# Kernel optimization log

Measured on AMD Instinct MI355X. Metric: run time of the kernel, lower is better.

## Reference

```python
import jax, jax.numpy as jnp
import numpy as np

B = 16
TOP_N = 4
IOU_THRESH = 0.25
PAD = 224
OUT = 224  # part image size
NUM_CLASSES = 200


def _gen_anchors(input_shape=(448, 448)):
    # Faithful port of NTSNet._generate_default_anchor_maps -> edge anchors,
    # then +PAD shift and int cast as in NTSNet.__init__.
    scales = [2.0 ** (1.0 / 3.0), 2.0 ** (2.0 / 3.0)]
    ratios = [0.667, 1.0, 1.5]
    settings = [(32, 48, scales), (64, 96, scales), (128, 192, [1.0] + scales)]
    edge = []
    for stride, size, scs in settings:
        H = int(np.ceil(input_shape[0] / stride))
        W = int(np.ceil(input_shape[1] / stride))
        ostart = stride / 2.0
        oy = np.arange(ostart, ostart + stride * H, stride).reshape(H, 1)
        ox = np.arange(ostart, ostart + stride * W, stride).reshape(1, W)
        cy = np.broadcast_to(oy, (H, W)).astype(np.float32)
        cx = np.broadcast_to(ox, (H, W)).astype(np.float32)
        for s in scs:
            for ar in ratios:
                h = size * s / float(ar) ** 0.5
                w = size * s * float(ar) ** 0.5
                e = np.stack([cy - h / 2.0, cx - w / 2.0, cy + h / 2.0, cx + w / 2.0], axis=-1)
                edge.append(e.reshape(-1, 4))
    edge = np.concatenate(edge, axis=0).astype(np.float32)
    return (edge + PAD).astype(np.int64).astype(np.int32)  # [1614,4] (y0,x0,y1,x1)


def _conv(x, w, b, stride, pad):
    y = jax.lax.conv_general_dilated(
        x, w, window_strides=(stride, stride),
        padding=[(pad, pad), (pad, pad)],
        dimension_numbers=("NCHW", "OIHW", "NCHW"))
    return y + b[None, :, None, None]


def _nms_single(scores, boxes, areas):
    # Hard NMS, fixed TOP_N iterations (jit-friendly): iteratively take the
    # highest-score box and suppress boxes with IoU >= IOU_THRESH.
    valid = jnp.ones(scores.shape, dtype=bool)
    picked = []
    for _ in range(TOP_N):
        i = jnp.argmax(jnp.where(valid, scores, -jnp.inf))
        b = boxes[i]
        ih = jnp.minimum(boxes[:, 2], b[2]) - jnp.maximum(boxes[:, 0], b[0])
        iw = jnp.minimum(boxes[:, 3], b[3]) - jnp.maximum(boxes[:, 1], b[1])
        inter = jnp.where((ih < 0) | (iw < 0), 0.0, ih * iw)
        iou = inter / (areas + areas[i] - inter)
        valid = valid & (iou < IOU_THRESH)
        picked.append(i)
    return jnp.stack(picked)  # [TOP_N]


def _crop_resize(img, box):
    # Bilinear resize of img[:, y0:y1, x0:x1] to OUTxOUT, align_corners=True
    # (matches F.interpolate(..., mode='bilinear', align_corners=True)).
    y0, x0, y1, x1 = box[0], box[1], box[2], box[3]
    h = (y1 - y0).astype(jnp.float32)
    w = (x1 - x0).astype(jnp.float32)
    t = jnp.arange(OUT, dtype=jnp.float32)
    sy = t * (h - 1.0) / (OUT - 1.0)
    sx = t * (w - 1.0) / (OUT - 1.0)
    fy = jnp.floor(sy)
    fx = jnp.floor(sx)
    wy = (sy - fy)[None, :, None]  # broadcast over rows
    wx = (sx - fx)[None, None, :]  # broadcast over cols
    iy0 = y0 + fy.astype(jnp.int32)
    ix0 = x0 + fx.astype(jnp.int32)
    iy1 = jnp.minimum(iy0 + 1, y1 - 1)
    ix1 = jnp.minimum(ix0 + 1, x1 - 1)
    r0 = img[:, iy0]  # [3,OUT,896]
    r1 = img[:, iy1]
    top = r0[:, :, ix0] * (1.0 - wx) + r0[:, :, ix1] * wx
    bot = r1[:, :, ix0] * (1.0 - wx) + r1[:, :, ix1] * wx
    return top * (1.0 - wy) + bot * wy  # [3,OUT,OUT]


def setup_inputs() -> dict:
    key = jax.random.key(0)
    ks = jax.random.split(key, 10)
    s = 0.02
    inp = {
        "x": jax.random.normal(ks[0], (B, 3, 448, 448), jnp.float32),
        "bb_w": jax.random.normal(ks[1], (2048, 3, 32, 32), jnp.float32) * s,
        "bb_b": jnp.zeros((2048,), jnp.float32),
        "n1_dw": jax.random.normal(ks[2], (128, 2048, 3, 3), jnp.float32) * s,
        "n1_db": jnp.zeros((128,), jnp.float32),
        "n1_tw": jax.random.normal(ks[3], (6, 128, 1, 1), jnp.float32) * s,
        "n1_tb": jnp.zeros((6,), jnp.float32),
        "n2_dw": jax.random.normal(ks[4], (128, 128, 3, 3), jnp.float32) * s,
        "n2_db": jnp.zeros((128,), jnp.float32),
        "n2_tw": jax.random.normal(ks[5], (6, 128, 1, 1), jnp.float32) * s,
        "n2_tb": jnp.zeros((6,), jnp.float32),
        "n3_dw": jax.random.normal(ks[6], (128, 128, 3, 3), jnp.float32) * s,
        "n3_db": jnp.zeros((128,), jnp.float32),
        "n3_tw": jax.random.normal(ks[7], (9, 128, 1, 1), jnp.float32) * s,
        "n3_tb": jnp.zeros((9,), jnp.float32),
        "cn_w": jax.random.normal(ks[8], (NUM_CLASSES, 10240), jnp.float32) * s,
        "cn_b": jnp.zeros((NUM_CLASSES,), jnp.float32),
        "anchors": jnp.asarray(_gen_anchors()),
    }
    return inp


def reference(x, bb_w, bb_b, n1_dw, n1_db, n1_tw, n1_tb, n2_dw, n2_db, n2_tw,
              n2_tb, n3_dw, n3_db, n3_tw, n3_tb, cn_w, cn_b, anchors):
    batch = x.shape[0]
    # Backbone -> raw pre-features [B,2048,14,14]
    raw = _conv(x, bb_w, bb_b, stride=32, pad=0)
    # Navigator unit -> rpn scores [B,1614]
    y1 = jax.nn.relu(_conv(raw, n1_dw, n1_db, 1, 1))            # [B,128,14,14]
    t1 = _conv(y1, n1_tw, n1_tb, 1, 0).reshape(batch, -1)        # [B,1176]
    y2 = jax.nn.relu(_conv(y1, n2_dw, n2_db, 2, 1))              # [B,128,7,7]
    t2 = _conv(y2, n2_tw, n2_tb, 1, 0).reshape(batch, -1)        # [B,294]
    y3 = jax.nn.relu(_conv(y2, n3_dw, n3_db, 2, 1))              # [B,128,4,4]
    t3 = _conv(y3, n3_tw, n3_tb, 1, 0).reshape(batch, -1)        # [B,144]
    rpn_score = jnp.concatenate([t1, t2, t3], axis=1)            # [B,1614]

    boxes_f = anchors.astype(jnp.float32)
    areas = (boxes_f[:, 2] - boxes_f[:, 0]) * (boxes_f[:, 3] - boxes_f[:, 1])
    top_idx = jax.vmap(_nms_single, in_axes=(0, None, None))(rpn_score, boxes_f, areas)  # [B,TOP_N]

    x_pad = jnp.pad(x, ((0, 0), (0, 0), (PAD, PAD), (PAD, PAD)))  # [B,3,896,896]
    sel_boxes = anchors[top_idx]                                  # [B,TOP_N,4]
    part_imgs = jax.vmap(lambda img, bs: jax.vmap(_crop_resize, in_axes=(None, 0))(img, bs))(
        x_pad, sel_boxes)                                         # [B,TOP_N,3,224,224]
    part_imgs = jax.lax.stop_gradient(part_imgs).reshape(batch * TOP_N, 3, OUT, OUT)

    # Shared backbone + tail (global avg pool; dropout is identity in eval)
    part_features = _conv(part_imgs, bb_w, bb_b, 32, 0).mean(axis=(2, 3))  # [B*TOP_N,2048]
    part_feature = part_features.reshape(batch, TOP_N, -1)[:, :4].reshape(batch, -1)  # num_cat=4
    raw_features = jax.lax.stop_gradient(raw).mean(axis=(2, 3))            # [B,2048]

    concat_out = jnp.concatenate([part_feature, raw_features], axis=1)     # [B,10240]
    concat_logits = concat_out @ cn_w.T + cn_b
    return concat_logits
```

## Files before the change

### kernel.cpp

```cpp
#include <hip/hip_runtime.h>
#include <cstdint>
#include <math.h>

typedef _Float16 half_t;
typedef __attribute__((ext_vector_type(8))) _Float16 half8;
typedef __attribute__((ext_vector_type(4))) float floatx4;


typedef __attribute__((address_space(3))) unsigned int lds_u32;
typedef const __attribute__((address_space(1))) unsigned int glb_u32;
__device__ __forceinline__ void glds16(const void* g, void* l) {
    __builtin_amdgcn_global_load_lds((glb_u32*)g, (lds_u32*)l, 16, 0, 0);
}

__global__ __launch_bounds__(256)
void prep_all(const float* __restrict__ x, const float* __restrict__ bbw,
              const float* __restrict__ n1dw, const float* __restrict__ n2dw,
              const float* __restrict__ n3dw, const float* __restrict__ cnb,
              const float* __restrict__ bbb,
              half_t* __restrict__ xh,
              half_t* __restrict__ bh, half_t* __restrict__ w1h,
              float* __restrict__ wt2t, float* __restrict__ wt3t,
              float* __restrict__ out, float* __restrict__ zpad,
              float* __restrict__ concat)
{
    const long t = (long)blockIdx.x * 256 + threadIdx.x;
    if (t < 1228800) {
        const int m = (int)(t % 3200), k8 = (int)(t / 3200);
        const int mt = m >> 7, mr = m & 127, s = k8 >> 2, kg = k8 & 3;
        const size_t dst = (((size_t)(mt * 96 + s) * 4 + kg) * 128 + mr) * 8;
        float f[8];
        if (m < 3136) {
            const int bq = m / 196, pos = m % 196, oy = pos / 14, ox = pos % 14;
            const int k = k8 * 8, c = k >> 10, r = (k >> 5) & 31, cc = k & 31;
            const float* p = x + ((size_t)(bq * 3 + c) * 448 + oy * 32 + r) * 448 + ox * 32 + cc;
            *(float4*)&f[0] = *(const float4*)p;
            *(float4*)&f[4] = *(const float4*)(p + 4);
        } else {
            #pragma unroll
            for (int j = 0; j < 8; ++j) f[j] = 0.f;
        }
        half8 h;
        #pragma unroll
        for (int j = 0; j < 8; ++j) h[j] = (half_t)f[j];
        *(half8*)(xh + dst) = h;
    } else if (t < 2015232) {
        const int t2 = (int)(t - 1228800);
        const int n = t2 / 384, k8 = t2 % 384;
        const float* p = bbw + (size_t)n * 3072 + k8 * 8;
        float f[8];
        *(float4*)&f[0] = *(const float4*)p;
        *(float4*)&f[4] = *(const float4*)(p + 4);
        const int nt = n >> 6, nr = n & 63, s = k8 >> 2, kg = k8 & 3;
        const size_t dst = (((size_t)(nt * 96 + s) * 4 + kg) * 64 + nr) * 8;
        half8 h;
        #pragma unroll
        for (int j = 0; j < 8; ++j) h[j] = (half_t)f[j];
        *(half8*)(bh + dst) = h;
    } else if (t < 2048000) {
        const int t2 = (int)(t - 2015232);
        const int n = t2 >> 8, ic8 = t2 & 255;
        const int s = ic8 >> 2, kg = ic8 & 3;
        const float* src = n1dw + ((size_t)n * 2048 + ic8 * 8) * 9;
        float buf[72];
        #pragma unroll
        for (int i = 0; i < 18; ++i) *(float4*)&buf[i * 4] = *(const float4*)(src + i * 4);
        #pragma unroll
        for (int tap = 0; tap < 9; ++tap) {
            half8 h;
            #pragma unroll
            for (int j = 0; j < 8; ++j) h[j] = (half_t)buf[j * 9 + tap];
            const size_t dst = (((size_t)(tap * 64 + s) * 4 + kg) * 128 + n) * 8;
            *(half8*)(w1h + dst) = h;
        }
    } else if (t < 2195456) {
        const int t2 = (int)(t - 2048000);
        const int oc = t2 % 128, rest = t2 / 128, ic = rest % 128, tap = rest / 128;
        wt2t[(tap * 128 + ic) * 128 + oc] = n2dw[((size_t)oc * 128 + ic) * 9 + tap];
    } else if (t < 2342912) {
        const int t2 = (int)(t - 2195456);
        const int oc = t2 % 128, rest = t2 / 128, ic = rest % 128, tap = rest / 128;
        wt3t[(tap * 128 + ic) * 128 + oc] = n3dw[((size_t)oc * 128 + ic) * 9 + tap];
    } else if (t < 2346112) {
        const int i = (int)(t - 2342912);
        out[i] = cnb[i % 200];
    } else if (t < 2346368) {
        zpad[t - 2346112] = 0.f;
    } else if (t < 2510208) {
        const int i = (int)(t - 2346368);
        const int r = i % 10240;
        concat[i] = (r < 8192) ? bbb[r & 2047] : 0.f;
    }
}

__global__ __launch_bounds__(256)
void gemm_x(const half_t* __restrict__ Ah, const half_t* __restrict__ Bh,
            const float* __restrict__ bias, half_t* __restrict__ outh)
{
    __shared__ __align__(16) char L[16384];
    const int tid = threadIdx.x, lane = tid & 63, wv = tid >> 6;
    const int nt = blockIdx.x, mt = blockIdx.y;
    const int lm = lane & 15, quad = lane >> 4;
    const int wm = wv >> 1, wn = wv & 1;

    const char* gAh = (const char*)Ah + (size_t)mt * 96 * 8192 + lane * 16;
    const int bhalf = wv >> 1, bkg = (wv & 1) * 2;
    const char* gB = (const char*)Bh + (size_t)(2 * nt + bhalf) * 96 * 4096 + bkg * 1024 + lane * 16;

    int afo[4], bfo[4];
    #pragma unroll
    for (int i = 0; i < 4; ++i) afo[i] = quad * 2048 + (wm * 64 + i * 16 + lm) * 16;
    #pragma unroll
    for (int j = 0; j < 4; ++j) bfo[j] = 8192 + wn * 4096 + quad * 1024 + (j * 16 + lm) * 16;

    floatx4 acc[4][4];
    const floatx4 fz = {0.f, 0.f, 0.f, 0.f};
    #pragma unroll
    for (int i = 0; i < 4; ++i)
        #pragma unroll
        for (int j = 0; j < 4; ++j) acc[i][j] = fz;

    for (int s = 0; s < 96; ++s) {
        const size_t sa = (size_t)s * 8192;
        glds16(gAh + sa + (2 * wv) * 1024,     L + (2 * wv) * 1024);
        glds16(gAh + sa + (2 * wv + 1) * 1024, L + (2 * wv + 1) * 1024);
        glds16(gB + (size_t)s * 4096,          L + 8192 + bhalf * 4096 + bkg * 1024);
        glds16(gB + (size_t)s * 4096 + 1024,   L + 8192 + bhalf * 4096 + (bkg + 1) * 1024);
        __syncthreads();
        half8 ah[4], bh[4];
        #pragma unroll
        for (int i = 0; i < 4; ++i) ah[i] = *(const half8*)(L + afo[i]);
        #pragma unroll
        for (int j = 0; j < 4; ++j) bh[j] = *(const half8*)(L + bfo[j]);
        #pragma unroll
        for (int i = 0; i < 4; ++i)
            #pragma unroll
            for (int j = 0; j < 4; ++j)
                acc[i][j] = __builtin_amdgcn_mfma_f32_16x16x32_f16(ah[i], bh[j], acc[i][j], 0, 0, 0);
        __syncthreads();
    }
    #pragma unroll
    for (int i = 0; i < 4; ++i) {
        const int m0 = mt * 128 + wm * 64 + i * 16 + quad * 4;
        #pragma unroll
        for (int j = 0; j < 4; ++j) {
            const int n = nt * 128 + wn * 64 + j * 16 + lm;
            const float bv = bias[n];
            #pragma unroll
            for (int r = 0; r < 4; ++r) {
                const int mm = m0 + r;
                if (mm < 3136)
                    outh[(size_t)mm * 2048 + n] = (half_t)(acc[i][j][r] + bv);
            }
        }
    }
}

__global__ __launch_bounds__(256)
void gemm_nav(const half_t* __restrict__ rawh, const half_t* __restrict__ Bh,
              const char* __restrict__ zpad, float* __restrict__ y1p)
{
    __shared__ __align__(16) char L[16384];
    const int tid = threadIdx.x, lane = tid & 63, wv = tid >> 6;
    const int tx = blockIdx.x;
    const int tap = tx >> 1, ks = tx & 1;
    const int mt = blockIdx.y;
    const int lm = lane & 15, quad = lane >> 4;
    const int wm = wv >> 1, wn = wv & 1;

    const char* baseH[2];
    int stp[2];
    #pragma unroll
    for (int rh = 0; rh < 2; ++rh) {
        const int grow = mt * 128 + rh * 64 + lane;
        const int b = grow / 196, pos = grow % 196, oy = pos / 14, ox = pos % 14;
        const int iy = oy + tap / 3 - 1, ix = ox + tap % 3 - 1;
        const bool av = (grow < 3136) && iy >= 0 && iy < 14 && ix >= 0 && ix < 14;
        const size_t rowoff = av ? ((size_t)(b * 196 + iy * 14 + ix)) * 4096 + ks * 2048 + wv * 16 : 0;
        baseH[rh] = av ? (const char*)rawh + rowoff : zpad;
        stp[rh] = av ? 64 : 0;
    }
    const char* gB = (const char*)Bh + (size_t)tap * 524288 + (size_t)ks * 32 * 8192 + lane * 16;

    int afo[4], bfo[4];
    #pragma unroll
    for (int i = 0; i < 4; ++i) afo[i] = quad * 2048 + (wm * 64 + i * 16 + lm) * 16;
    #pragma unroll
    for (int j = 0; j < 4; ++j) bfo[j] = 8192 + quad * 2048 + (wn * 64 + j * 16 + lm) * 16;

    floatx4 acc[4][4];
    const floatx4 fz = {0.f, 0.f, 0.f, 0.f};
    #pragma unroll
    for (int i = 0; i < 4; ++i)
        #pragma unroll
        for (int j = 0; j < 4; ++j) acc[i][j] = fz;

    for (int s = 0; s < 32; ++s) {
        glds16(baseH[0] + s * stp[0], L + wv * 2048);
        glds16(baseH[1] + s * stp[1], L + wv * 2048 + 1024);
        glds16(gB + (size_t)s * 8192 + (2 * wv) * 1024,     L + 8192 + (2 * wv) * 1024);
        glds16(gB + (size_t)s * 8192 + (2 * wv + 1) * 1024, L + 8192 + (2 * wv + 1) * 1024);
        __syncthreads();
        half8 ah[4], bh[4];
        #pragma unroll
        for (int i = 0; i < 4; ++i) ah[i] = *(const half8*)(L + afo[i]);
        #pragma unroll
        for (int j = 0; j < 4; ++j) bh[j] = *(const half8*)(L + bfo[j]);
        #pragma unroll
        for (int i = 0; i < 4; ++i)
            #pragma unroll
            for (int j = 0; j < 4; ++j)
                acc[i][j] = __builtin_amdgcn_mfma_f32_16x16x32_f16(ah[i], bh[j], acc[i][j], 0, 0, 0);
        __syncthreads();
    }
    #pragma unroll
    for (int i = 0; i < 4; ++i) {
        const int m0 = mt * 128 + wm * 64 + i * 16 + quad * 4;
        #pragma unroll
        for (int j = 0; j < 4; ++j) {
            const int n = wn * 64 + j * 16 + lm;
            #pragma unroll
            for (int r = 0; r < 4; ++r) {
                const int mm = m0 + r;
                if (mm < 3136)
                    y1p[((size_t)tx * 3136 + mm) * 128 + n] = acc[i][j][r];
            }
        }
    }
}

__global__ __launch_bounds__(256)
void y1r_rm(const float* __restrict__ y1p, const float* __restrict__ bias,
            float* __restrict__ y1,
            const half_t* __restrict__ rh, float* __restrict__ concat)
{
    if (blockIdx.x < 1568) {
        const int t = blockIdx.x * 256 + threadIdx.x;
        const int n = t & 127;
        float s = bias[n];
        #pragma unroll
        for (int ks = 0; ks < 18; ++ks) s += y1p[(size_t)ks * 3136 * 128 + t];
        y1[t] = fmaxf(s, 0.f);
    } else {
        const int t = (blockIdx.x - 1568) * 256 + threadIdx.x;
        const int n = t & 2047, b = (t >> 11) & 15, pc = t >> 15;
        float s = 0.f;
        const int p0 = pc * 49;
        for (int p = p0; p < p0 + 49; ++p)
            s += (float)rh[(size_t)(b * 196 + p) * 2048 + n];
        atomicAdd(concat + (size_t)b * 10240 + 8192 + n, s * (1.f / 196.f));
    }
}

__global__ __launch_bounds__(256)
void tidy_all(const float* __restrict__ y1, const float* __restrict__ y2,
              const float* __restrict__ y3,
              const float* __restrict__ w1, const float* __restrict__ b1,
              const float* __restrict__ w2, const float* __restrict__ b2,
              const float* __restrict__ w3, const float* __restrict__ b3,
              float* __restrict__ scores)
{
    const int wid = (blockIdx.x * 256 + threadIdx.x) >> 6;
    const int lane = threadIdx.x & 63;
    if (wid >= 16 * 1614) return;
    const int b = wid / 1614, idx = wid % 1614;
    const float* in; const float* w; const float* bi; int ch;
    if (idx < 1176) {
        ch = idx / 196; in = y1 + (size_t)(b * 196 + idx % 196) * 128; w = w1; bi = b1;
    } else if (idx < 1470) {
        const int i2 = idx - 1176;
        ch = i2 / 49; in = y2 + (size_t)(b * 49 + i2 % 49) * 128; w = w2; bi = b2;
    } else {
        const int i3 = idx - 1470;
        ch = i3 / 16; in = y3 + (size_t)(b * 16 + i3 % 16) * 128; w = w3; bi = b3;
    }
    const float* wr = w + ch * 128;
    float acc = in[lane] * wr[lane] + in[lane + 64] * wr[lane + 64];
    #pragma unroll
    for (int s = 32; s > 0; s >>= 1) acc += __shfl_down(acc, s, 64);
    if (lane == 0) scores[b * 1614 + idx] = acc + bi[ch];
}

__global__ __launch_bounds__(256)
void conv_s2(const float* __restrict__ in, const float* __restrict__ wt,
             const float* __restrict__ bias, float* __restrict__ out,
             int Win, int Wout)
{
    const int t = blockIdx.x * 256 + threadIdx.x;
    const int oc = t & 127;
    const int pos = (t >> 7) % (Wout * Wout);
    const int b = t / (128 * Wout * Wout);
    if (b >= 16) return;
    const int oy = pos / Wout, ox = pos % Wout;
    float acc = bias[oc];
    for (int dy = 0; dy < 3; ++dy) {
        const int y = oy * 2 + dy - 1;
        if (y < 0 || y >= Win) continue;
        for (int dx = 0; dx < 3; ++dx) {
            const int x = ox * 2 + dx - 1;
            if (x < 0 || x >= Win) continue;
            const float* ip = in + (size_t)(b * Win * Win + y * Win + x) * 128;
            const float* wp = wt + (size_t)(dy * 3 + dx) * 16384 + oc;
            for (int ic = 0; ic < 128; ++ic)
                acc += ip[ic] * wp[ic * 128];
        }
    }
    out[(size_t)(b * Wout * Wout + pos) * 128 + oc] = fmaxf(acc, 0.f);
}

__global__ __launch_bounds__(256)
void nms(const float* __restrict__ scores, const int* __restrict__ anchors,
         int* __restrict__ top_idx)
{
    __shared__ float wv_v[4];
    __shared__ int wv_i[4];
    __shared__ int s_pick;
    const int b = blockIdx.x, tid = threadIdx.x;
    const int lane = tid & 63, wv = tid >> 6;
    float sc[7], ay0[7], ax0[7], ay1[7], ax1[7];
    unsigned int vmask = 0;
    #pragma unroll
    for (int j = 0; j < 7; ++j) {
        const int i = tid + j * 256;
        if (i < 1614) {
            sc[j]  = scores[b * 1614 + i];
            ay0[j] = (float)anchors[i * 4 + 0];
            ax0[j] = (float)anchors[i * 4 + 1];
            ay1[j] = (float)anchors[i * 4 + 2];
            ax1[j] = (float)anchors[i * 4 + 3];
            vmask |= 1u << j;
        }
    }
    for (int r = 0; r < 4; ++r) {
        float bv = -INFINITY; int bi = 0x7fffffff;
        #pragma unroll
        for (int j = 0; j < 7; ++j) {
            if (vmask & (1u << j)) {
                const float v = sc[j];
                const int i = tid + j * 256;
                if (v > bv || (v == bv && i < bi)) { bv = v; bi = i; }
            }
        }
        #pragma unroll
        for (int s = 32; s > 0; s >>= 1) {
            const float v2 = __shfl_down(bv, s, 64);
            const int   i2 = __shfl_down(bi, s, 64);
            if (v2 > bv || (v2 == bv && i2 < bi)) { bv = v2; bi = i2; }
        }
        if (lane == 0) { wv_v[wv] = bv; wv_i[wv] = bi; }
        __syncthreads();
        if (tid == 0) {
            float fv = wv_v[0]; int fi = wv_i[0];
            #pragma unroll
            for (int k = 1; k < 4; ++k)
                if (wv_v[k] > fv || (wv_v[k] == fv && wv_i[k] < fi)) { fv = wv_v[k]; fi = wv_i[k]; }
            s_pick = fi;
            top_idx[b * 4 + r] = fi;
        }
        __syncthreads();
        const int pick = s_pick;
        const float py0 = (float)anchors[pick * 4 + 0], px0 = (float)anchors[pick * 4 + 1];
        const float py1 = (float)anchors[pick * 4 + 2], px1 = (float)anchors[pick * 4 + 3];
        const float pa = (py1 - py0) * (px1 - px0);
        #pragma unroll
        for (int j = 0; j < 7; ++j) {
            if (vmask & (1u << j)) {
                const float ih = fminf(ay1[j], py1) - fmaxf(ay0[j], py0);
                const float iw = fminf(ax1[j], px1) - fmaxf(ax0[j], px0);
                const float inter = (ih < 0.f || iw < 0.f) ? 0.f : ih * iw;
                const float area = (ay1[j] - ay0[j]) * (ax1[j] - ax0[j]);
                const float iou = inter / ((area + pa) - inter);
                if (iou >= 0.25f) vmask &= ~(1u << j);
            }
        }
    }
}

__global__ __launch_bounds__(256)
void crop_mean(const float* __restrict__ x, const int* __restrict__ anchors,
               const int* __restrict__ top_idx, float* __restrict__ abar)
{
    __shared__ float red[256];
    const int bi = blockIdx.x;
    const int q = bi / 96, rem = bi % 96, c = rem >> 5, r = rem & 31;
    const int tid = threadIdx.x;
    const int cc = tid & 31, ps = tid >> 5;
    const int idx = top_idx[q];
    const int y0 = anchors[idx * 4 + 0], x0 = anchors[idx * 4 + 1];
    const int y1 = anchors[idx * 4 + 2], x1 = anchors[idx * 4 + 3];
    const float hh = (float)(y1 - y0), ww = (float)(x1 - x0);
    const float* xb = x + (size_t)((q >> 2) * 3 + c) * 200704;
    float acc = 0.f;
    for (int p = ps; p < 49; p += 8) {
        const int oy = p / 7, ox = p % 7;
        const int typ = oy * 32 + r;
        const int txp = ox * 32 + cc;
        const float sy = (float)typ * (hh - 1.0f) / 223.0f;
        const float fy = floorf(sy);
        const float wy = sy - fy;
        const int iy0 = y0 + (int)fy;
        const int iy1 = min(iy0 + 1, y1 - 1);
        const float sx = (float)txp * (ww - 1.0f) / 223.0f;
        const float fx = floorf(sx);
        const float wx = sx - fx;
        const int ix0 = x0 + (int)fx;
        const int ix1 = min(ix0 + 1, x1 - 1);
        const int ry0 = iy0 - 224, ry1 = iy1 - 224;
        const int rx0 = ix0 - 224, rx1 = ix1 - 224;
        const bool vy0 = (ry0 >= 0 && ry0 < 448), vy1 = (ry1 >= 0 && ry1 < 448);
        const bool vx0 = (rx0 >= 0 && rx0 < 448), vx1 = (rx1 >= 0 && rx1 < 448);
        const float v00 = (vy0 && vx0) ? xb[(size_t)ry0 * 448 + rx0] : 0.f;
        const float v01 = (vy0 && vx1) ? xb[(size_t)ry0 * 448 + rx1] : 0.f;
        const float v10 = (vy1 && vx0) ? xb[(size_t)ry1 * 448 + rx0] : 0.f;
        const float v11 = (vy1 && vx1) ? xb[(size_t)ry1 * 448 + rx1] : 0.f;
        const float top = v00 * (1.f - wx) + v01 * wx;
        const float bot = v10 * (1.f - wx) + v11 * wx;
        acc += top * (1.f - wy) + bot * wy;
    }
    red[tid] = acc;
    __syncthreads();
    if (tid < 32) {
        float s = 0.f;
        #pragma unroll
        for (int k = 0; k < 8; ++k) s += red[tid + 32 * k];
        abar[(size_t)q * 3072 + c * 1024 + r * 32 + cc] = s * (1.f / 49.f);
    }
}

__global__ __launch_bounds__(256)
void part_gemm(const float* __restrict__ abar, const half_t* __restrict__ Bh,
               float* __restrict__ concat)
{
    __shared__ __align__(16) char L[12288];
    const int tid = threadIdx.x, lane = tid & 63, wv = tid >> 6;
    const int lm = lane & 15, quad = lane >> 4;
    const int nt = blockIdx.x, ks = blockIdx.y;
    const char* gBh = (const char*)Bh + ((size_t)nt * 96 + ks * 12) * 4096 + lane * 16;
    const int am = tid & 63, akg = tid >> 6;

    floatx4 acc[4], accl[4];
    const floatx4 fz = {0.f, 0.f, 0.f, 0.f};
    #pragma unroll
    for (int j = 0; j < 4; ++j) { acc[j] = fz; accl[j] = fz; }

    for (int s = 0; s < 12; ++s) {
        {
            const float* pa = abar + (size_t)am * 3072 + (ks * 12 + s) * 32 + akg * 8;
            float f[8];
            *(float4*)&f[0] = *(const float4*)pa;
            *(float4*)&f[4] = *(const float4*)(pa + 4);
            half8 h, l;
            #pragma unroll
            for (int j = 0; j < 8; ++j) {
                const half_t hh = (half_t)f[j];
                h[j] = hh;
                l[j] = (half_t)(f[j] - (float)hh);
            }
            *(half8*)(L + (akg * 64 + am) * 16) = h;
            *(half8*)(L + 4096 + (akg * 64 + am) * 16) = l;
        }
        glds16(gBh + (size_t)s * 4096 + wv * 1024, L + 8192 + wv * 1024);
        __syncthreads();
        half8 ah, al, bh[4];
        ah = *(const half8*)(L + (quad * 64 + wv * 16 + lm) * 16);
        al = *(const half8*)(L + 4096 + (quad * 64 + wv * 16 + lm) * 16);
        #pragma unroll
        for (int j = 0; j < 4; ++j) bh[j] = *(const half8*)(L + 8192 + (quad * 64 + j * 16 + lm) * 16);
        #pragma unroll
        for (int j = 0; j < 4; ++j) {
            acc[j]  = __builtin_amdgcn_mfma_f32_16x16x32_f16(ah, bh[j], acc[j], 0, 0, 0);
            accl[j] = __builtin_amdgcn_mfma_f32_16x16x32_f16(al, bh[j], accl[j], 0, 0, 0);
        }
        __syncthreads();
    }
    #pragma unroll
    for (int j = 0; j < 4; ++j) {
        const int n = nt * 64 + j * 16 + lm;
        #pragma unroll
        for (int r = 0; r < 4; ++r) {
            const int m = wv * 16 + quad * 4 + r;
            atomicAdd(concat + (size_t)(m >> 2) * 10240 + (m & 3) * 2048 + n,
                      acc[j][r] + accl[j][r]);
        }
    }
}

__global__ __launch_bounds__(256)
void cls_gemm(const float* __restrict__ concat, const float* __restrict__ w,
              float* __restrict__ out)
{
    __shared__ float ws_[8 * 321];
    __shared__ float cs_[16 * 321];
    __shared__ float red[256];
    const int nchunk = blockIdx.x, ks = blockIdx.y;
    const int tid = threadIdx.x;
    for (int i = tid; i < 2560; i += 256) {
        const int r = i / 320, k = i % 320;
        ws_[r * 321 + k] = w[(size_t)(nchunk * 8 + r) * 10240 + ks * 320 + k];
    }
    for (int i = tid; i < 5120; i += 256) {
        const int r = i / 320, k = i % 320;
        cs_[r * 321 + k] = concat[(size_t)r * 10240 + ks * 320 + k];
    }
    __syncthreads();
    const int b = tid & 15, c = (tid >> 4) & 7, hf = tid >> 7;
    const float* cp = cs_ + b * 321 + hf * 160;
    const float* wp = ws_ + c * 321 + hf * 160;
    float a = 0.f;
    #pragma unroll 8
    for (int k = 0; k < 160; ++k) a += cp[k] * wp[k];
    red[tid] = a;
    __syncthreads();
    if (tid < 128) atomicAdd(out + b * 200 + nchunk * 8 + c, red[tid] + red[tid + 128]);
}

extern "C" void kernel_launch(void* const* d_in, const int* in_sizes, int n_in,
                              void* d_out, int out_size, void* d_ws, size_t ws_size,
                              hipStream_t stream)
{
    const float* x     = (const float*)d_in[0];
    const float* bb_w  = (const float*)d_in[1];
    const float* bb_b  = (const float*)d_in[2];
    const float* n1_dw = (const float*)d_in[3];
    const float* n1_db = (const float*)d_in[4];
    const float* n1_tw = (const float*)d_in[5];
    const float* n1_tb = (const float*)d_in[6];
    const float* n2_dw = (const float*)d_in[7];
    const float* n2_db = (const float*)d_in[8];
    const float* n2_tw = (const float*)d_in[9];
    const float* n2_tb = (const float*)d_in[10];
    const float* n3_dw = (const float*)d_in[11];
    const float* n3_db = (const float*)d_in[12];
    const float* n3_tw = (const float*)d_in[13];
    const float* n3_tb = (const float*)d_in[14];
    const float* cn_w  = (const float*)d_in[15];
    const float* cn_b  = (const float*)d_in[16];
    const int*   anchors = (const int*)d_in[17];
    float* out = (float*)d_out;
    char* W = (char*)d_ws;

    half_t* bbwh  = (half_t*)(W + 0);
    float*  zpad  = (float*)(W + 12582912);
    int*    topidx= (int*)(W + 12583936);
    float*  scores= (float*)(W + 12584960);
    float*  y1    = (float*)(W + 12688384);
    float*  y2    = (float*)(W + 14294016);
    float*  y3    = (float*)(W + 14695424);
    float*  concat= (float*)(W + 14826496);
    half_t* w1h   = (half_t*)(W + 15481856);
    float*  wt2t  = (float*)(W + 20200448);
    float*  wt3t  = (float*)(W + 20790272);
    char* E = W + 21380096;
    half_t* xh    = (half_t*)E;
    float*  y1p   = (float*)E;
    char* F = W + 60701696;
    half_t* rawh  = (half_t*)F;
    float*  abar  = (float*)F;

    prep_all<<<9806, 256, 0, stream>>>(x, bb_w, n1_dw, n2_dw, n3_dw, cn_b, bb_b,
                                       xh, bbwh, w1h, wt2t, wt3t, out, zpad, concat);

    gemm_x<<<dim3(16, 25), 256, 0, stream>>>(xh, bbwh, bb_b, rawh);
    gemm_nav<<<dim3(18, 25), 256, 0, stream>>>(rawh, w1h, (const char*)zpad, y1p);
    y1r_rm<<<2080, 256, 0, stream>>>(y1p, n1_db, y1, rawh, concat);

    conv_s2<<<392, 256, 0, stream>>>(y1, wt2t, n2_db, y2, 14, 7);
    conv_s2<<<128, 256, 0, stream>>>(y2, wt3t, n3_db, y3, 7, 4);
    tidy_all<<<6456, 256, 0, stream>>>(y1, y2, y3, n1_tw, n1_tb, n2_tw, n2_tb,
                                       n3_tw, n3_tb, scores);

    nms<<<16, 256, 0, stream>>>(scores, anchors, topidx);
    crop_mean<<<6144, 256, 0, stream>>>(x, anchors, topidx, abar);

    part_gemm<<<dim3(32, 8), 256, 0, stream>>>(abar, bbwh, concat);
    cls_gemm<<<dim3(25, 32), 256, 0, stream>>>(concat, cn_w, out);
}
```

Baseline: 409.6 us.

## Shrink GEMM M-tile to 64 rows and fuse tidy scoring into stride-2 convs

Both the backbone GEMM and the navigator 3x3 GEMM move from 128x128 tiles to 64x128 tiles, with each wave owning 16 rows and 8 N-fragments. Each iteration now covers two K-steps of MFMA with a larger LDS buffer. Since 3136 = 49*64, the grids grow from 25 to 49 M-tiles, which gives more blocks to spread across CUs and drops the row-bound checks. Separately, the per-scale tidy score dot products are folded into the conv kernels and a small tidy3 kernel. This lets score work overlap with the convs instead of running after all of them, at the cost of less per-block operand reuse in the GEMMs.

```diff
diff --git a/kernel.cpp b/kernel.cpp
--- a/kernel.cpp
+++ b/kernel.cpp
@@ -97,62 +97,56 @@
 void gemm_x(const half_t* __restrict__ Ah, const half_t* __restrict__ Bh,
             const float* __restrict__ bias, half_t* __restrict__ outh)
 {
-    __shared__ __align__(16) char L[16384];
+    __shared__ __align__(16) char L[24576];
     const int tid = threadIdx.x, lane = tid & 63, wv = tid >> 6;
     const int nt = blockIdx.x, mt = blockIdx.y;
     const int lm = lane & 15, quad = lane >> 4;
-    const int wm = wv >> 1, wn = wv & 1;
-
-    const char* gAh = (const char*)Ah + (size_t)mt * 96 * 8192 + lane * 16;
-    const int bhalf = wv >> 1, bkg = (wv & 1) * 2;
-    const char* gB = (const char*)Bh + (size_t)(2 * nt + bhalf) * 96 * 4096 + bkg * 1024 + lane * 16;
-
-    int afo[4], bfo[4];
-    #pragma unroll
-    for (int i = 0; i < 4; ++i) afo[i] = quad * 2048 + (wm * 64 + i * 16 + lm) * 16;
-    #pragma unroll
-    for (int j = 0; j < 4; ++j) bfo[j] = 8192 + wn * 4096 + quad * 1024 + (j * 16 + lm) * 16;
-
-    floatx4 acc[4][4];
+
+    const char* gA = (const char*)Ah + (size_t)(mt >> 1) * 786432 + (mt & 1) * 1024 + lane * 16;
+    const char* gB = (const char*)Bh + (size_t)(2 * nt) * 393216 + lane * 16;
+
+    const int a0 = 2 * wv, a1 = 2 * wv + 1;
+    const int aof0 = (a0 >> 2) * 4096 + (a0 & 3) * 1024;
+    const int aog0 = (a0 >> 2) * 8192 + (a0 & 3) * 2048;
+    const int aof1 = (a1 >> 2) * 4096 + (a1 & 3) * 1024;
+    const int aog1 = (a1 >> 2) * 8192 + (a1 & 3) * 2048;
+    const int bsi = wv >> 1, bnh = wv & 1;
+    const size_t bgb = (size_t)bnh * 393216 + bsi * 4096;
+    const int blb = 8192 + (bsi * 2 + bnh) * 4096;
+
+    floatx4 acc[8];
     const floatx4 fz = {0.f, 0.f, 0.f, 0.f};
     #pragma unroll
-    for (int i = 0; i < 4; ++i)
-        #pragma unroll
-        for (int j = 0; j < 4; ++j) acc[i][j] = fz;
-
-    for (int s = 0; s < 96; ++s) {
-        const size_t sa = (size_t)s * 8192;
-        glds16(gAh + sa + (2 * wv) * 1024,     L + (2 * wv) * 1024);
-        glds16(gAh + sa + (2 * wv + 1) * 1024, L + (2 * wv + 1) * 1024);
-        glds16(gB + (size_t)s * 4096,          L + 8192 + bhalf * 4096 + bkg * 1024);
-        glds16(gB + (size_t)s * 4096 + 1024,   L + 8192 + bhalf * 4096 + (bkg + 1) * 1024);
-        __syncthreads();
-        half8 ah[4], bh[4];
-        #pragma unroll
-        for (int i = 0; i < 4; ++i) ah[i] = *(const half8*)(L + afo[i]);
-        #pragma unroll
-        for (int j = 0; j < 4; ++j) bh[j] = *(const half8*)(L + bfo[j]);
+    for (int j = 0; j < 8; ++j) acc[j] = fz;
+
+    for (int s = 0; s < 48; ++s) {
+        const size_t sa = (size_t)(2 * s) * 8192;
+        const size_t sb = (size_t)(2 * s) * 4096;
+        glds16(gA + sa + aog0, L + aof0);
+        glds16(gA + sa + aog1, L + aof1);
         #pragma unroll
         for (int i = 0; i < 4; ++i)
+            glds16(gB + bgb + sb + i * 1024, L + blb + i * 1024);
+        __syncthreads();
+        #pragma unroll
+        for (int ki = 0; ki < 2; ++ki) {
+            half8 a = *(const half8*)(L + ki * 4096 + quad * 1024 + (wv * 16 + lm) * 16);
             #pragma unroll
-            for (int j = 0; j < 4; ++j)
-                acc[i][j] = __builtin_amdgcn_mfma_f32_16x16x32_f16(ah[i], bh[j], acc[i][j], 0, 0, 0);
-        __syncthreads();
-    }
-    #pragma unroll
-    for (int i = 0; i < 4; ++i) {
-        const int m0 = mt * 128 + wm * 64 + i * 16 + quad * 4;
-        #pragma unroll
-        for (int j = 0; j < 4; ++j) {
-            const int n = nt * 128 + wn * 64 + j * 16 + lm;
-            const float bv = bias[n];
-            #pragma unroll
-            for (int r = 0; r < 4; ++r) {
-                const int mm = m0 + r;
-                if (mm < 3136)
-                    outh[(size_t)mm * 2048 + n] = (half_t)(acc[i][j][r] + bv);
+            for (int j = 0; j < 8; ++j) {
+                half8 b = *(const half8*)(L + 8192 + (ki * 2 + (j >> 2)) * 4096 + quad * 1024 + ((j & 3) * 16 + lm) * 16);
+                acc[j] = __builtin_amdgcn_mfma_f32_16x16x32_f16(a, b, acc[j], 0, 0, 0);
             }
         }
+        __syncthreads();
+    }
+    const int m0 = mt * 64 + wv * 16 + quad * 4;
+    #pragma unroll
+    for (int j = 0; j < 8; ++j) {
+        const int n = nt * 128 + j * 16 + lm;
+        const float bv = bias[n];
+        #pragma unroll
+        for (int r = 0; r < 4; ++r)
+            outh[(size_t)(m0 + r) * 2048 + n] = (half_t)(acc[j][r] + bv);
     }
 }
 
@@ -160,72 +154,59 @@
 void gemm_nav(const half_t* __restrict__ rawh, const half_t* __restrict__ Bh,
               const char* __restrict__ zpad, float* __restrict__ y1p)
 {
-    __shared__ __align__(16) char L[16384];
+    __shared__ __align__(16) char L[24576];
     const int tid = threadIdx.x, lane = tid & 63, wv = tid >> 6;
     const int tx = blockIdx.x;
     const int tap = tx >> 1, ks = tx & 1;
     const int mt = blockIdx.y;
     const int lm = lane & 15, quad = lane >> 4;
-    const int wm = wv >> 1, wn = wv & 1;
-
-    const char* baseH[2];
-    int stp[2];
-    #pragma unroll
-    for (int rh = 0; rh < 2; ++rh) {
-        const int grow = mt * 128 + rh * 64 + lane;
-        const int b = grow / 196, pos = grow % 196, oy = pos / 14, ox = pos % 14;
-        const int iy = oy + tap / 3 - 1, ix = ox + tap % 3 - 1;
-        const bool av = (grow < 3136) && iy >= 0 && iy < 14 && ix >= 0 && ix < 14;
-        const size_t rowoff = av ? ((size_t)(b * 196 + iy * 14 + ix)) * 4096 + ks * 2048 + wv * 16 : 0;
-        baseH[rh] = av ? (const char*)rawh + rowoff : zpad;
-        stp[rh] = av ? 64 : 0;
-    }
-    const char* gB = (const char*)Bh + (size_t)tap * 524288 + (size_t)ks * 32 * 8192 + lane * 16;
-
-    int afo[4], bfo[4];
-    #pragma unroll
-    for (int i = 0; i < 4; ++i) afo[i] = quad * 2048 + (wm * 64 + i * 16 + lm) * 16;
-    #pragma unroll
-    for (int j = 0; j < 4; ++j) bfo[j] = 8192 + quad * 2048 + (wn * 64 + j * 16 + lm) * 16;
-
-    floatx4 acc[4][4];
+
+    const int grow = mt * 64 + lane;
+    const int b = grow / 196, pos = grow % 196, oy = pos / 14, ox = pos % 14;
+    const int iy = oy + tap / 3 - 1, ix = ox + tap % 3 - 1;
+    const bool av = (iy >= 0 && iy < 14 && ix >= 0 && ix < 14);
+    const char* abase = av ? (const char*)rawh + ((size_t)(b * 196 + iy * 14 + ix)) * 4096 + ks * 2048 : zpad;
+    const int stp = av ? 1 : 0;
+
+    const int a0 = 2 * wv, a1 = 2 * wv + 1;
+    const int ac0 = (a0 >> 2) * 64 + (a0 & 3) * 16, al0 = (a0 >> 2) * 4096 + (a0 & 3) * 1024;
+    const int ac1 = (a1 >> 2) * 64 + (a1 & 3) * 16, al1 = (a1 >> 2) * 4096 + (a1 & 3) * 1024;
+    const int bsi = wv >> 1, bnh = wv & 1;
+    const char* gB = (const char*)Bh + (size_t)tap * 524288 + (size_t)(ks * 32) * 8192 + bnh * 1024 + lane * 16;
+    const int blb = 8192 + bsi * 8192 + bnh * 1024;
+
+    floatx4 acc[8];
     const floatx4 fz = {0.f, 0.f, 0.f, 0.f};
     #pragma unroll
-    for (int i = 0; i < 4; ++i)
-        #pragma unroll
-        for (int j = 0; j < 4; ++j) acc[i][j] = fz;
-
-    for (int s = 0; s < 32; ++s) {
-        glds16(baseH[0] + s * stp[0], L + wv * 2048);
-        glds16(baseH[1] + s * stp[1], L + wv * 2048 + 1024);
-        glds16(gB + (size_t)s * 8192 + (2 * wv) * 1024,     L + 8192 + (2 * wv) * 1024);
-        glds16(gB + (size_t)s * 8192 + (2 * wv + 1) * 1024, L + 8192 + (2 * wv + 1) * 1024);
-        __syncthreads();
-        half8 ah[4], bh[4];
-        #pragma unroll
-        for (int i = 0; i < 4; ++i) ah[i] = *(const half8*)(L + afo[i]);
-        #pragma unroll
-        for (int j = 0; j < 4; ++j) bh[j] = *(const half8*)(L + bfo[j]);
+    for (int j = 0; j < 8; ++j) acc[j] = fz;
+
+    for (int s = 0; s < 16; ++s) {
+        const int rowo = s * 128;
+        glds16(abase + stp * (rowo + ac0), L + al0);
+        glds16(abase + stp * (rowo + ac1), L + al1);
+        const size_t sb = (size_t)(2 * s + bsi) * 8192;
         #pragma unroll
         for (int i = 0; i < 4; ++i)
+            glds16(gB + sb + i * 2048, L + blb + i * 2048);
+        __syncthreads();
+        #pragma unroll
+        for (int ki = 0; ki < 2; ++ki) {
+            half8 a = *(const half8*)(L + ki * 4096 + quad * 1024 + (wv * 16 + lm) * 16);
             #pragma unroll
-            for (int j = 0; j < 4; ++j)
-                acc[i][j] = __builtin_amdgcn_mfma_f32_16x16x32_f16(ah[i], bh[j], acc[i][j], 0, 0, 0);
-        __syncthreads();
-    }
-    #pragma unroll
-    for (int i = 0; i < 4; ++i) {
-        const int m0 = mt * 128 + wm * 64 + i * 16 + quad * 4;
-        #pragma unroll
-        for (int j = 0; j < 4; ++j) {
-            const int n = wn * 64 + j * 16 + lm;
-            #pragma unroll
-            for (int r = 0; r < 4; ++r) {
-                const int mm = m0 + r;
-                if (mm < 3136)
-                    y1p[((size_t)tx * 3136 + mm) * 128 + n] = acc[i][j][r];
+            for (int j = 0; j < 8; ++j) {
+                half8 bq = *(const half8*)(L + 8192 + ki * 8192 + quad * 2048 + (j * 16 + lm) * 16);
+                acc[j] = __builtin_amdgcn_mfma_f32_16x16x32_f16(a, bq, acc[j], 0, 0, 0);
             }
         }
+        __syncthreads();
+    }
+    const int m0 = mt * 64 + wv * 16 + quad * 4;
+    #pragma unroll
+    for (int j = 0; j < 8; ++j) {
+        const int n = j * 16 + lm;
+        #pragma unroll
+        for (int r = 0; r < 4; ++r)
+            y1p[((size_t)tx * 3136 + m0 + r) * 128 + n] = acc[j][r];
     }
 }
 
@@ -252,41 +233,20 @@
     }
 }
 
-__global__ __launch_bounds__(256)
-void tidy_all(const float* __restrict__ y1, const float* __restrict__ y2,
-              const float* __restrict__ y3,
-              const float* __restrict__ w1, const float* __restrict__ b1,
-              const float* __restrict__ w2, const float* __restrict__ b2,
-              const float* __restrict__ w3, const float* __restrict__ b3,
-              float* __restrict__ scores)
-{
-    const int wid = (blockIdx.x * 256 + threadIdx.x) >> 6;
-    const int lane = threadIdx.x & 63;
-    if (wid >= 16 * 1614) return;
-    const int b = wid / 1614, idx = wid % 1614;
-    const float* in; const float* w; const float* bi; int ch;
-    if (idx < 1176) {
-        ch = idx / 196; in = y1 + (size_t)(b * 196 + idx % 196) * 128; w = w1; bi = b1;
-    } else if (idx < 1470) {
-        const int i2 = idx - 1176;
-        ch = i2 / 49; in = y2 + (size_t)(b * 49 + i2 % 49) * 128; w = w2; bi = b2;
-    } else {
-        const int i3 = idx - 1470;
-        ch = i3 / 16; in = y3 + (size_t)(b * 16 + i3 % 16) * 128; w = w3; bi = b3;
-    }
-    const float* wr = w + ch * 128;
+__device__ __forceinline__ void tidy_one(const float* in, const float* wr, float bi,
+                                         float* dst, int lane)
+{
     float acc = in[lane] * wr[lane] + in[lane + 64] * wr[lane + 64];
     #pragma unroll
     for (int s = 32; s > 0; s >>= 1) acc += __shfl_down(acc, s, 64);
-    if (lane == 0) scores[b * 1614 + idx] = acc + bi[ch];
-}
-
-__global__ __launch_bounds__(256)
-void conv_s2(const float* __restrict__ in, const float* __restrict__ wt,
-             const float* __restrict__ bias, float* __restrict__ out,
-             int Win, int Wout)
-{
-    const int t = blockIdx.x * 256 + threadIdx.x;
+    if (lane == 0) *dst = acc + bi;
+}
+
+__device__ __forceinline__ void conv_s2_body(int t, const float* __restrict__ in,
+                                             const float* __restrict__ wt,
+                                             const float* __restrict__ bias,
+                                             float* __restrict__ out, int Win, int Wout)
+{
     const int oc = t & 127;
     const int pos = (t >> 7) % (Wout * Wout);
     const int b = t / (128 * Wout * Wout);
@@ -306,6 +266,57 @@
         }
     }
     out[(size_t)(b * Wout * Wout + pos) * 128 + oc] = fmaxf(acc, 0.f);
+}
+
+__global__ __launch_bounds__(256)
+void conv2_tidy1(const float* __restrict__ y1, const float* __restrict__ wt2t,
+                 const float* __restrict__ b2d, float* __restrict__ y2,
+                 const float* __restrict__ w1t, const float* __restrict__ b1t,
+                 float* __restrict__ scores)
+{
+    if (blockIdx.x < 392) {
+        conv_s2_body(blockIdx.x * 256 + threadIdx.x, y1, wt2t, b2d, y2, 14, 7);
+    } else {
+        const int wid = (blockIdx.x - 392) * 4 + (threadIdx.x >> 6);
+        const int lane = threadIdx.x & 63;
+        if (wid >= 16 * 1176) return;
+        const int b = wid / 1176, i1 = wid % 1176;
+        const int ch = i1 / 196, pos = i1 % 196;
+        tidy_one(y1 + (size_t)(b * 196 + pos) * 128, w1t + ch * 128, b1t[ch],
+                 scores + b * 1614 + i1, lane);
+    }
+}
+
+__global__ __launch_bounds__(256)
+void conv3_tidy2(const float* __restrict__ y2, const float* __restrict__ wt3t,
+                 const float* __restrict__ b3d, float* __restrict__ y3,
+                 const float* __restrict__ w2t, const float* __restrict__ b2t,
+                 float* __restrict__ scores)
+{
+    if (blockIdx.x < 128) {
+        conv_s2_body(blockIdx.x * 256 + threadIdx.x, y2, wt3t, b3d, y3, 7, 4);
+    } else {
+        const int wid = (blockIdx.x - 128) * 4 + (threadIdx.x >> 6);
+        const int lane = threadIdx.x & 63;
+        if (wid >= 16 * 294) return;
+        const int b = wid / 294, i2 = wid % 294;
+        const int ch = i2 / 49, pos = i2 % 49;
+        tidy_one(y2 + (size_t)(b * 49 + pos) * 128, w2t + ch * 128, b2t[ch],
+                 scores + b * 1614 + 1176 + i2, lane);
+    }
+}
+
+__global__ __launch_bounds__(256)
+void tidy3(const float* __restrict__ y3, const float* __restrict__ w3t,
+           const float* __restrict__ b3t, float* __restrict__ scores)
+{
+    const int wid = blockIdx.x * 4 + (threadIdx.x >> 6);
+    const int lane = threadIdx.x & 63;
+    if (wid >= 16 * 144) return;
+    const int b = wid / 144, i3 = wid % 144;
+    const int ch = i3 / 16, pos = i3 % 16;
+    tidy_one(y3 + (size_t)(b * 16 + pos) * 128, w3t + ch * 128, b3t[ch],
+             scores + b * 1614 + 1470 + i3, lane);
 }
 
 __global__ __launch_bounds__(256)
@@ -560,14 +571,13 @@
     prep_all<<<9806, 256, 0, stream>>>(x, bb_w, n1_dw, n2_dw, n3_dw, cn_b, bb_b,
                                        xh, bbwh, w1h, wt2t, wt3t, out, zpad, concat);
 
-    gemm_x<<<dim3(16, 25), 256, 0, stream>>>(xh, bbwh, bb_b, rawh);
-    gemm_nav<<<dim3(18, 25), 256, 0, stream>>>(rawh, w1h, (const char*)zpad, y1p);
+    gemm_x<<<dim3(16, 49), 256, 0, stream>>>(xh, bbwh, bb_b, rawh);
+    gemm_nav<<<dim3(18, 49), 256, 0, stream>>>(rawh, w1h, (const char*)zpad, y1p);
     y1r_rm<<<2080, 256, 0, stream>>>(y1p, n1_db, y1, rawh, concat);
 
-    conv_s2<<<392, 256, 0, stream>>>(y1, wt2t, n2_db, y2, 14, 7);
-    conv_s2<<<128, 256, 0, stream>>>(y2, wt3t, n3_db, y3, 7, 4);
-    tidy_all<<<6456, 256, 0, stream>>>(y1, y2, y3, n1_tw, n1_tb, n2_tw, n2_tb,
-                                       n3_tw, n3_tb, scores);
+    conv2_tidy1<<<5096, 256, 0, stream>>>(y1, wt2t, n2_db, y2, n1_tw, n1_tb, scores);
+    conv3_tidy2<<<1304, 256, 0, stream>>>(y2, wt3t, n3_db, y3, n2_tw, n2_tb, scores);
+    tidy3<<<576, 256, 0, stream>>>(y3, n3_tw, n3_tb, scores);
 
     nms<<<16, 256, 0, stream>>>(scores, anchors, topidx);
     crop_mean<<<6144, 256, 0, stream>>>(x, anchors, topidx, abar);
```

Result: faster. 393.7 us (-3.9%).
